# Performance work log

Hardware: AMD Instinct MI355X
Metric: run time of the kernel (lower is better)

Reference implementation:

```python
import jax, jax.numpy as jnp
import numpy as np

EPS = 1e-3  # Keras BatchNormalization default epsilon


def _binarize(x):
    # sign() binarization with straight-through estimator (identity gradient)
    b = jnp.where(x >= 0, 1.0, -1.0).astype(x.dtype)
    return x + jax.lax.stop_gradient(b - x)


def _conv(x, w):
    # NHWC input, HWIO kernel, stride 1, 'same' padding
    return jax.lax.conv_general_dilated(
        x, w, (1, 1), 'SAME', dimension_numbers=('NHWC', 'HWIO', 'NHWC'))


def _bn(x, p):
    # p: [4, C] rows = gamma, beta, moving_mean, moving_var (inference BN)
    gamma, beta, mean, var = p[0], p[1], p[2], p[3]
    return gamma * (x - mean) * jax.lax.rsqrt(var + EPS) + beta


def _maxpool(x):
    return jax.lax.reduce_window(x, -jnp.inf, jax.lax.max,
                                 (1, 2, 2, 1), (1, 2, 2, 1), 'VALID')


def _bconv_block(x, w, bn_p):
    # BinaryConv2D(activation='relu', use_bias=False) -> BatchNormalization
    y = jax.nn.relu(_conv(_binarize(x), _binarize(w)))
    return _bn(y, bn_p)


def setup_inputs() -> dict:
    key = jax.random.key(0)
    ks = iter(jax.random.split(key, 64))

    def w(shape, scale=0.05):
        return jax.random.normal(next(ks), shape, jnp.float32) * scale

    def bn_params(c):
        gamma = 1.0 + 0.1 * jax.random.normal(next(ks), (c,), jnp.float32)
        beta = 0.1 * jax.random.normal(next(ks), (c,), jnp.float32)
        mean = 0.1 * jax.random.normal(next(ks), (c,), jnp.float32)
        var = 0.5 + jax.random.uniform(next(ks), (c,), jnp.float32)
        return jnp.stack([gamma, beta, mean, var])

    inp = {
        'inputs': jax.random.normal(next(ks), (16, 224, 224, 3), jnp.float32),
        'conv1_w': w((3, 3, 3, 64)), 'conv1_b': w((64,)), 'bn1': bn_params(64),
        'w2': w((3, 3, 64, 128)),  'bn2': bn_params(128),
        'w3': w((3, 3, 128, 256)), 'bn3': bn_params(256),
        'w4': w((3, 3, 256, 256)), 'bn4': bn_params(256),
        'w5': w((3, 3, 256, 512)), 'bn5': bn_params(512),
        'w6': w((3, 3, 512, 512)), 'bn6': bn_params(512),
        'w7': w((3, 3, 512, 512)), 'bn7': bn_params(512),
        'w8': w((3, 3, 512, 512)), 'bn8': bn_params(512),
        'dense_w': w((512, 1000)),
    }
    return inp


def reference(inputs, conv1_w, conv1_b, bn1, w2, bn2, w3, bn3, w4, bn4,
              w5, bn5, w6, bn6, w7, bn7, w8, bn8, dense_w):
    # stage 1: full-precision conv -> BN -> maxpool
    x = jax.nn.relu(_conv(inputs, conv1_w) + conv1_b)
    x = _bn(x, bn1)
    x = _maxpool(x)              # 224 -> 112
    x = 0.5 * x                  # Scale(0.5)
    # binary (XNOR) conv stages, stride 1 (use_maxpool=True)
    x = _bconv_block(x, w2, bn2)
    x = _maxpool(x)              # 112 -> 56
    x = _bconv_block(x, w3, bn3)
    x = _bconv_block(x, w4, bn4)
    x = _maxpool(x)              # 56 -> 28
    x = _bconv_block(x, w5, bn5)
    x = _bconv_block(x, w6, bn6)
    x = _maxpool(x)              # 28 -> 14
    x = _bconv_block(x, w7, bn7)
    x = _bconv_block(x, w8, bn8)
    x = _maxpool(x)              # 14 -> 7
    x = jnp.mean(x, axis=(1, 2))  # global average pool -> [B, 512]
    # BinaryDense: binarized input and weights, no bias
    return _binarize(x) @ _binarize(dense_w)
```

## Files before the change

kernel.cpp:

```cpp
#include <hip/hip_runtime.h>
#include <cstdint>

using u64 = unsigned long long;

__global__ void pack_conv_weights(const float* __restrict__ w, u64* __restrict__ wb,
                                  int Cin, int Cout) {
    int cinw = Cin >> 6;
    int total = 9 * cinw * Cout;
    int idx = blockIdx.x * blockDim.x + threadIdx.x;
    if (idx >= total) return;
    int co = idx % Cout;
    int rest = idx / Cout;
    int wd = rest % cinw;
    int t = rest / cinw;
    u64 word = 0ull;
    for (int b = 0; b < 64; ++b) {
        int ci = (wd << 6) + b;
        float v = w[(t * Cin + ci) * Cout + co];
        if (v >= 0.f) word |= (1ull << b);
    }
    wb[idx] = word;
}

__global__ void pack_dense_weights(const float* __restrict__ w, u64* __restrict__ wb) {
    int j = blockIdx.x * blockDim.x + threadIdx.x;
    if (j >= 1000) return;
    for (int wd = 0; wd < 8; ++wd) {
        u64 word = 0ull;
        for (int b = 0; b < 64; ++b) {
            float v = w[((wd << 6) + b) * 1000 + j];
            if (v >= 0.f) word |= (1ull << b);
        }
        wb[j * 8 + wd] = word;
    }
}

__global__ void prep_bnthr(const float* __restrict__ bn, int cout,
                           double* __restrict__ thrd, int* __restrict__ sflag) {
    int i = blockIdx.x * blockDim.x + threadIdx.x;
    if (i >= cout) return;
    double g  = (double)bn[i];
    double be = (double)bn[cout + i];
    double mu = (double)bn[2 * cout + i];
    double va = (double)bn[3 * cout + i];
    double s  = g * (1.0 / sqrt(va + 1e-3));
    thrd[i] = mu - be / s;
    sflag[i] = (s >= 0.0) ? 1 : 0;
}

__global__ void prep_thrf(const double* __restrict__ thrd, float* __restrict__ thrf) {
    int i = threadIdx.x;
    if (i < 64) thrf[i] = (float)thrd[i];
}

__global__ __launch_bounds__(256, 1)
void conv1_fused(const float* __restrict__ in, const float* __restrict__ w,
                 const float* __restrict__ bias,
                 const float* __restrict__ thrf, const double* __restrict__ thrd,
                 const int* __restrict__ sflag,
                 u64* __restrict__ outbits) {
    int lane = threadIdx.x & 63;
    int wid = blockIdx.x * (blockDim.x >> 6) + (threadIdx.x >> 6);
    int pxq = wid % 28;
    int py  = (wid / 28) % 112;
    int n   = wid / (28 * 112);

    float  thrv = thrf[lane];
    double thrD = thrd[lane];
    bool   spos = (sflag[lane] != 0);
    float  bif  = bias[lane];

    float wreg[27];
#pragma unroll
    for (int t = 0; t < 9; ++t)
#pragma unroll
        for (int c = 0; c < 3; ++c)
            wreg[t * 3 + c] = w[(t * 3 + c) * 64 + lane];

    const float TAU = 2e-4f;
    int iy0 = 2 * py - 1;
    bool rowint = (py >= 1) & (py <= 110);

#pragma unroll 1
    for (int pp = 0; pp < 4; ++pp) {
        int px = 4 * pxq + pp;
        int ix0 = 2 * px - 1;

        float patch[4][12];
        bool interior = rowint & (px >= 1) & (px <= 110);
        if (interior) {
            const float* base = in + ((size_t)(n * 224 + iy0) * 224 + ix0) * 3;
#pragma unroll
            for (int r = 0; r < 4; ++r) {
                const float* rp = base + (size_t)r * (224 * 3);
#pragma unroll
                for (int c = 0; c < 12; ++c) patch[r][c] = rp[c];
            }
        } else {
#pragma unroll
            for (int r = 0; r < 4; ++r) {
                int iy = iy0 + r;
                bool rv = (iy >= 0) & (iy < 224);
#pragma unroll
                for (int cc = 0; cc < 4; ++cc) {
                    int ix = ix0 + cc;
                    bool v = rv & (ix >= 0) & (ix < 224);
                    const float* p = in + ((size_t)(n * 224 + iy) * 224 + ix) * 3;
#pragma unroll
                    for (int c = 0; c < 3; ++c)
                        patch[r][cc * 3 + c] = v ? p[c] : 0.f;
                }
            }
        }

        bool pred = false;
#pragma unroll
        for (int q = 0; q < 4; ++q) {
            int qy = q >> 1, qx = q & 1;
            float accf = bif;
#pragma unroll
            for (int dy = 0; dy < 3; ++dy)
#pragma unroll
                for (int dx = 0; dx < 3; ++dx)
#pragma unroll
                    for (int c = 0; c < 3; ++c)
                        accf = fmaf(patch[qy + dy][(qx + dx) * 3 + c],
                                    wreg[(dy * 3 + dx) * 3 + c], accf);
            float rf = fmaxf(accf, 0.f);
            bool p = spos ? (rf >= thrv) : (rf <= thrv);
            if (fabsf(rf - thrv) < TAU) {
                double acc = (double)bif;
#pragma unroll
                for (int dy = 0; dy < 3; ++dy)
#pragma unroll
                    for (int dx = 0; dx < 3; ++dx)
#pragma unroll
                        for (int c = 0; c < 3; ++c)
                            acc = fma((double)patch[qy + dy][(qx + dx) * 3 + c],
                                      (double)wreg[(dy * 3 + dx) * 3 + c], acc);
                double rd = fmax(acc, 0.0);
                p = spos ? (rd >= thrD) : (rd <= thrD);
            }
            pred |= p;
        }
        u64 word = __ballot(pred);
        if (lane == 0) outbits[((size_t)(n * 112 + py)) * 112 + px] = word;
    }
}

template<int CINW, int COUT, int P, bool OUTF64>
__global__ void bconv(const u64* __restrict__ xin, const u64* __restrict__ wb,
                      const float* __restrict__ bn,
                      const double* __restrict__ thrd, const int* __restrict__ sflag,
                      u64* __restrict__ obits, double* __restrict__ of64,
                      int H, int W) {
    constexpr int CW = COUT >> 6;
    __shared__ u64 sh[3][P + 2][CINW];

    int tid = threadIdx.x;
    int XT = (W + P - 1) / P;
    int pos = blockIdx.x;
    int xt = pos % XT;
    int yy = (pos / XT) % H;
    int n  = pos / (XT * H);
    int x0 = xt * P;

    for (int i = tid; i < 3 * (P + 2) * CINW; i += COUT) {
        int wd = i % CINW;
        int cc = (i / CINW) % (P + 2);
        int rr = i / (CINW * (P + 2));
        int gy = yy - 1 + rr, gx = x0 - 1 + cc;
        u64 v = 0ull;
        if (gy >= 0 && gy < H && gx >= 0 && gx < W)
            v = xin[((size_t)(n * H + gy) * W + gx) * CINW + wd];
        sh[rr][cc][wd] = v;
    }
    __syncthreads();

    int acc[P];
#pragma unroll
    for (int p = 0; p < P; ++p) acc[p] = 0;

    int co = tid;
    bool leftv  = (x0 > 0);
    bool rightv = (x0 + P < W);

    for (int dy = 0; dy < 3; ++dy) {
        int gy = yy - 1 + dy;
        if (gy < 0 || gy >= H) continue;
#pragma unroll 1
        for (int w = 0; w < CINW; ++w) {
            u64 w0 = wb[((dy * 3 + 0) * CINW + w) * COUT + co];
            u64 w1 = wb[((dy * 3 + 1) * CINW + w) * COUT + co];
            u64 w2 = wb[((dy * 3 + 2) * CINW + w) * COUT + co];
#pragma unroll
            for (int c = 0; c < P + 2; ++c) {
                if (c == 0 && !leftv) continue;
                if (c == P + 1 && !rightv) continue;
                u64 v = sh[dy][c][w];
                if (c < P)  acc[c]     += __popcll(v ^ w0);
                if (c >= 1 && c <= P) acc[c - 1] += __popcll(v ^ w1);
                if (c >= 2) acc[c - 2] += __popcll(v ^ w2);
            }
        }
    }

    int ndy = 3 - (yy == 0) - (yy == H - 1);
    int lane = tid & 63, wv = tid >> 6;

    if constexpr (OUTF64) {
        double g  = (double)bn[co];
        double be = (double)bn[COUT + co];
        double mu = (double)bn[2 * COUT + co];
        double va = (double)bn[3 * COUT + co];
        double rsq = 1.0 / sqrt(va + 1e-3);
#pragma unroll
        for (int p = 0; p < P; ++p) {
            int x = x0 + p;
            bool eL = (x == 0), eR = (x == W - 1);
            int nvp = ndy * (3 - eL - eR);
            int y = nvp * (CINW * 64) - 2 * acc[p];
            int yr = y > 0 ? y : 0;
            double v = g * ((double)yr - mu) * rsq + be;
            if (x < W) of64[((size_t)(n * H + yy) * W + x) * COUT + co] = v;
        }
    } else {
        double thr = thrd[co];
        bool spos = (sflag[co] != 0);
#pragma unroll
        for (int p = 0; p < P; ++p) {
            int x = x0 + p;
            bool eL = (x == 0), eR = (x == W - 1);
            int nvp = ndy * (3 - eL - eR);
            int y = nvp * (CINW * 64) - 2 * acc[p];
            int yr = y > 0 ? y : 0;
            double yd = (double)yr;
            bool pred = spos ? (yd >= thr) : (yd <= thr);
            u64 word = __ballot(pred);
            if (lane == 0 && x < W)
                obits[((size_t)(n * H + yy) * W + x) * CW + wv] = word;
        }
    }
}

__global__ void pool_bits(const u64* __restrict__ in, u64* __restrict__ out,
                          int H2, int W2, int CW) {
    int idx = blockIdx.x * blockDim.x + threadIdx.x;
    int total = 16 * H2 * W2 * CW;
    if (idx >= total) return;
    int wd = idx % CW;
    int rest = idx / CW;
    int px = rest % W2; rest /= W2;
    int py = rest % H2;
    int n = rest / H2;
    int W = 2 * W2;
    const u64* base = in + ((size_t)(n * 2 * H2 + 2 * py) * W + 2 * px) * CW + wd;
    out[idx] = base[0] | base[CW] | base[(size_t)W * CW] | base[(size_t)W * CW + CW];
}

__global__ void gap_part(const double* __restrict__ x, double* __restrict__ part) {
    int b = blockIdx.x;
    int py = b % 7, n = b / 7;
    int co = threadIdx.x;
    double sum = 0.0;
    for (int px = 0; px < 7; ++px) {
        const double* bp = x + ((size_t)(n * 14 + 2 * py) * 14 + 2 * px) * 512 + co;
        double m = bp[0];
        m = fmax(m, bp[512]);
        m = fmax(m, bp[14 * 512]);
        m = fmax(m, bp[14 * 512 + 512]);
        sum += m;
    }
    part[((size_t)n * 7 + py) * 512 + co] = sum;
}

__global__ void gap_final(const double* __restrict__ part, u64* __restrict__ gb) {
    int n = blockIdx.x;
    int co = threadIdx.x;
    double sum = 0.0;
    for (int py = 0; py < 7; ++py) sum += part[((size_t)n * 7 + py) * 512 + co];
    double mean = sum / 49.0;
    bool pred = (mean >= 0.0);
    u64 word = __ballot(pred);
    if ((co & 63) == 0) gb[n * 8 + (co >> 6)] = word;
}

__global__ void dense_bin(const u64* __restrict__ gb, const u64* __restrict__ dwb,
                          float* __restrict__ out) {
    int idx = blockIdx.x * blockDim.x + threadIdx.x;
    if (idx >= 16000) return;
    int j = idx % 1000, n = idx / 1000;
    const u64* g = gb + n * 8;
    const u64* w = dwb + j * 8;
    int acc = 0;
#pragma unroll
    for (int wd = 0; wd < 8; ++wd) acc += __popcll(g[wd] ^ w[wd]);
    out[idx] = (float)(512 - 2 * acc);
}

extern "C" void kernel_launch(void* const* d_in, const int* in_sizes, int n_in,
                              void* d_out, int out_size, void* d_ws, size_t ws_size,
                              hipStream_t stream) {
    const float* inputs = (const float*)d_in[0];
    const float* w1  = (const float*)d_in[1];
    const float* b1  = (const float*)d_in[2];
    const float* bn1 = (const float*)d_in[3];
    const float* w2  = (const float*)d_in[4];
    const float* bn2 = (const float*)d_in[5];
    const float* w3  = (const float*)d_in[6];
    const float* bn3 = (const float*)d_in[7];
    const float* w4  = (const float*)d_in[8];
    const float* bn4 = (const float*)d_in[9];
    const float* w5  = (const float*)d_in[10];
    const float* bn5 = (const float*)d_in[11];
    const float* w6  = (const float*)d_in[12];
    const float* bn6 = (const float*)d_in[13];
    const float* w7  = (const float*)d_in[14];
    const float* bn7 = (const float*)d_in[15];
    const float* w8  = (const float*)d_in[16];
    const float* bn8 = (const float*)d_in[17];
    const float* dw  = (const float*)d_in[18];
    float* out = (float*)d_out;

    u64* ws = (u64*)d_ws;
    size_t o = 0;
    auto alloc = [&](size_t n) { u64* p = ws + o; o += n; return p; };

    u64* wb2 = alloc(9 * 1 * 128);
    u64* wb3 = alloc(9 * 2 * 256);
    u64* wb4 = alloc(9 * 4 * 256);
    u64* wb5 = alloc(9 * 4 * 512);
    u64* wb6 = alloc(9 * 8 * 512);
    u64* wb7 = alloc(9 * 8 * 512);
    u64* wb8 = alloc(9 * 8 * 512);
    u64* dwb = alloc(1000 * 8);

    double* th1 = (double*)alloc(64);   int* sf1 = (int*)alloc(64);
    double* th2 = (double*)alloc(128);  int* sf2 = (int*)alloc(128);
    double* th3 = (double*)alloc(256);  int* sf3 = (int*)alloc(256);
    double* th4 = (double*)alloc(256);  int* sf4 = (int*)alloc(256);
    double* th5 = (double*)alloc(512);  int* sf5 = (int*)alloc(512);
    double* th6 = (double*)alloc(512);  int* sf6 = (int*)alloc(512);
    double* th7 = (double*)alloc(512);  int* sf7 = (int*)alloc(512);
    float*  tf1 = (float*)alloc(64);

    u64* x2b = alloc(16 * 112 * 112 * 1);
    u64* c2b = alloc(16 * 112 * 112 * 2);
    u64* x3b = alloc(16 * 56 * 56 * 2);
    u64* c3b = alloc(16 * 56 * 56 * 4);
    u64* c4b = alloc(16 * 56 * 56 * 4);
    u64* x5b = alloc(16 * 28 * 28 * 4);
    u64* c5b = alloc(16 * 28 * 28 * 8);
    u64* c6b = alloc(16 * 28 * 28 * 8);
    u64* x7b = alloc(16 * 14 * 14 * 8);
    u64* c7b = alloc(16 * 14 * 14 * 8);
    u64* gb  = alloc(16 * 8);
    double* c8f   = (double*)alloc(16 * 14 * 14 * 512);
    double* gpart = (double*)alloc(16 * 7 * 512);

    auto grid = [](int n, int b) { return (n + b - 1) / b; };
    pack_conv_weights<<<grid(9 * 1 * 128, 256), 256, 0, stream>>>(w2, wb2, 64, 128);
    pack_conv_weights<<<grid(9 * 2 * 256, 256), 256, 0, stream>>>(w3, wb3, 128, 256);
    pack_conv_weights<<<grid(9 * 4 * 256, 256), 256, 0, stream>>>(w4, wb4, 256, 256);
    pack_conv_weights<<<grid(9 * 4 * 512, 256), 256, 0, stream>>>(w5, wb5, 256, 512);
    pack_conv_weights<<<grid(9 * 8 * 512, 256), 256, 0, stream>>>(w6, wb6, 512, 512);
    pack_conv_weights<<<grid(9 * 8 * 512, 256), 256, 0, stream>>>(w7, wb7, 512, 512);
    pack_conv_weights<<<grid(9 * 8 * 512, 256), 256, 0, stream>>>(w8, wb8, 512, 512);
    pack_dense_weights<<<4, 256, 0, stream>>>(dw, dwb);

    prep_bnthr<<<1, 64, 0, stream>>>(bn1, 64, th1, sf1);
    prep_bnthr<<<1, 128, 0, stream>>>(bn2, 128, th2, sf2);
    prep_bnthr<<<1, 256, 0, stream>>>(bn3, 256, th3, sf3);
    prep_bnthr<<<1, 256, 0, stream>>>(bn4, 256, th4, sf4);
    prep_bnthr<<<grid(512, 256), 256, 0, stream>>>(bn5, 512, th5, sf5);
    prep_bnthr<<<grid(512, 256), 256, 0, stream>>>(bn6, 512, th6, sf6);
    prep_bnthr<<<grid(512, 256), 256, 0, stream>>>(bn7, 512, th7, sf7);
    prep_thrf<<<1, 64, 0, stream>>>(th1, tf1);

    conv1_fused<<<16 * 112 * 28 / 4, 256, 0, stream>>>(inputs, w1, b1, tf1, th1, sf1, x2b);

    bconv<1, 128, 8, false><<<16 * 112 * 14, 128, 0, stream>>>(x2b, wb2, bn2, th2, sf2, c2b, nullptr, 112, 112);
    pool_bits<<<grid(16 * 56 * 56 * 2, 256), 256, 0, stream>>>(c2b, x3b, 56, 56, 2);
    bconv<2, 256, 8, false><<<16 * 56 * 7, 256, 0, stream>>>(x3b, wb3, bn3, th3, sf3, c3b, nullptr, 56, 56);
    bconv<4, 256, 8, false><<<16 * 56 * 7, 256, 0, stream>>>(c3b, wb4, bn4, th4, sf4, c4b, nullptr, 56, 56);
    pool_bits<<<grid(16 * 28 * 28 * 4, 256), 256, 0, stream>>>(c4b, x5b, 28, 28, 4);
    bconv<4, 512, 7, false><<<16 * 28 * 4, 512, 0, stream>>>(x5b, wb5, bn5, th5, sf5, c5b, nullptr, 28, 28);
    bconv<8, 512, 7, false><<<16 * 28 * 4, 512, 0, stream>>>(c5b, wb6, bn6, th6, sf6, c6b, nullptr, 28, 28);
    pool_bits<<<grid(16 * 14 * 14 * 8, 256), 256, 0, stream>>>(c6b, x7b, 14, 14, 8);
    bconv<8, 512, 7, false><<<16 * 14 * 2, 512, 0, stream>>>(x7b, wb7, bn7, th7, sf7, c7b, nullptr, 14, 14);
    bconv<8, 512, 7, true><<<16 * 14 * 2, 512, 0, stream>>>(c7b, wb8, bn8, nullptr, nullptr, nullptr, c8f, 14, 14);

    gap_part<<<16 * 7, 512, 0, stream>>>(c8f, gpart);
    gap_final<<<16, 512, 0, stream>>>(gpart, gb);
    dense_bin<<<grid(16000, 256), 256, 0, stream>>>(gb, dwb, out);
}
```

Baseline: 518.4 us.

## Register-block binary conv over two output rows to reuse weight loads

The binary conv kernel now computes R=2 output rows per block, staging R+2 input rows in shared memory and loading all nine weight words per input word once, then reusing them across both rows. This halves the number of weight global loads per output and halves the block count. In exchange it doubles the accumulator registers and the shared tile, which may reduce occupancy. It also assumes H and W divide evenly by R and P, so the x<W guards are dropped.

```diff
diff --git a/kernel.cpp b/kernel.cpp
--- a/kernel.cpp
+++ b/kernel.cpp
@@ -148,28 +148,30 @@
     }
 }
 
-template<int CINW, int COUT, int P, bool OUTF64>
+template<int CINW, int COUT, int P, int R, bool OUTF64>
 __global__ void bconv(const u64* __restrict__ xin, const u64* __restrict__ wb,
                       const float* __restrict__ bn,
                       const double* __restrict__ thrd, const int* __restrict__ sflag,
                       u64* __restrict__ obits, double* __restrict__ of64,
                       int H, int W) {
     constexpr int CW = COUT >> 6;
-    __shared__ u64 sh[3][P + 2][CINW];
+    __shared__ u64 sh[R + 2][P + 2][CINW];
 
     int tid = threadIdx.x;
-    int XT = (W + P - 1) / P;
+    int XT = W / P;
+    int YT = H / R;
     int pos = blockIdx.x;
     int xt = pos % XT;
-    int yy = (pos / XT) % H;
-    int n  = pos / (XT * H);
+    int yt = (pos / XT) % YT;
+    int n  = pos / (XT * YT);
     int x0 = xt * P;
-
-    for (int i = tid; i < 3 * (P + 2) * CINW; i += COUT) {
+    int y0 = yt * R;
+
+    for (int i = tid; i < (R + 2) * (P + 2) * CINW; i += COUT) {
         int wd = i % CINW;
         int cc = (i / CINW) % (P + 2);
         int rr = i / (CINW * (P + 2));
-        int gy = yy - 1 + rr, gx = x0 - 1 + cc;
+        int gy = y0 - 1 + rr, gx = x0 - 1 + cc;
         u64 v = 0ull;
         if (gy >= 0 && gy < H && gx >= 0 && gx < W)
             v = xin[((size_t)(n * H + gy) * W + gx) * CINW + wd];
@@ -177,35 +179,44 @@
     }
     __syncthreads();
 
-    int acc[P];
-#pragma unroll
-    for (int p = 0; p < P; ++p) acc[p] = 0;
+    int acc[R][P];
+#pragma unroll
+    for (int r = 0; r < R; ++r)
+#pragma unroll
+        for (int p = 0; p < P; ++p) acc[r][p] = 0;
 
     int co = tid;
     bool leftv  = (x0 > 0);
     bool rightv = (x0 + P < W);
 
-    for (int dy = 0; dy < 3; ++dy) {
-        int gy = yy - 1 + dy;
-        if (gy < 0 || gy >= H) continue;
 #pragma unroll 1
-        for (int w = 0; w < CINW; ++w) {
-            u64 w0 = wb[((dy * 3 + 0) * CINW + w) * COUT + co];
-            u64 w1 = wb[((dy * 3 + 1) * CINW + w) * COUT + co];
-            u64 w2 = wb[((dy * 3 + 2) * CINW + w) * COUT + co];
+    for (int w = 0; w < CINW; ++w) {
+        u64 wt[9];
+#pragma unroll
+        for (int t = 0; t < 9; ++t)
+            wt[t] = wb[(t * CINW + w) * COUT + co];
+#pragma unroll
+        for (int rr = 0; rr < R + 2; ++rr) {
+            int gy = y0 + rr - 1;
+            if (gy < 0 || gy >= H) continue;
 #pragma unroll
             for (int c = 0; c < P + 2; ++c) {
                 if (c == 0 && !leftv) continue;
                 if (c == P + 1 && !rightv) continue;
-                u64 v = sh[dy][c][w];
-                if (c < P)  acc[c]     += __popcll(v ^ w0);
-                if (c >= 1 && c <= P) acc[c - 1] += __popcll(v ^ w1);
-                if (c >= 2) acc[c - 2] += __popcll(v ^ w2);
-            }
-        }
-    }
-
-    int ndy = 3 - (yy == 0) - (yy == H - 1);
+                u64 v = sh[rr][c][w];
+#pragma unroll
+                for (int r = 0; r < R; ++r) {
+                    constexpr int unused = 0; (void)unused;
+                    int dy = rr - r;
+                    if (dy < 0 || dy > 2) continue;
+                    if (c < P)            acc[r][c]     += __popcll(v ^ wt[dy * 3 + 0]);
+                    if (c >= 1 && c <= P) acc[r][c - 1] += __popcll(v ^ wt[dy * 3 + 1]);
+                    if (c >= 2)           acc[r][c - 2] += __popcll(v ^ wt[dy * 3 + 2]);
+                }
+            }
+        }
+    }
+
     int lane = tid & 63, wv = tid >> 6;
 
     if constexpr (OUTF64) {
@@ -215,30 +226,40 @@
         double va = (double)bn[3 * COUT + co];
         double rsq = 1.0 / sqrt(va + 1e-3);
 #pragma unroll
-        for (int p = 0; p < P; ++p) {
-            int x = x0 + p;
-            bool eL = (x == 0), eR = (x == W - 1);
-            int nvp = ndy * (3 - eL - eR);
-            int y = nvp * (CINW * 64) - 2 * acc[p];
-            int yr = y > 0 ? y : 0;
-            double v = g * ((double)yr - mu) * rsq + be;
-            if (x < W) of64[((size_t)(n * H + yy) * W + x) * COUT + co] = v;
+        for (int r = 0; r < R; ++r) {
+            int yy = y0 + r;
+            int ndy = 3 - (yy == 0) - (yy == H - 1);
+#pragma unroll
+            for (int p = 0; p < P; ++p) {
+                int x = x0 + p;
+                bool eL = (x == 0), eR = (x == W - 1);
+                int nvp = ndy * (3 - eL - eR);
+                int y = nvp * (CINW * 64) - 2 * acc[r][p];
+                int yr = y > 0 ? y : 0;
+                double v = g * ((double)yr - mu) * rsq + be;
+                of64[((size_t)(n * H + yy) * W + x) * COUT + co] = v;
+            }
         }
     } else {
         double thr = thrd[co];
         bool spos = (sflag[co] != 0);
 #pragma unroll
-        for (int p = 0; p < P; ++p) {
-            int x = x0 + p;
-            bool eL = (x == 0), eR = (x == W - 1);
-            int nvp = ndy * (3 - eL - eR);
-            int y = nvp * (CINW * 64) - 2 * acc[p];
-            int yr = y > 0 ? y : 0;
-            double yd = (double)yr;
-            bool pred = spos ? (yd >= thr) : (yd <= thr);
-            u64 word = __ballot(pred);
-            if (lane == 0 && x < W)
-                obits[((size_t)(n * H + yy) * W + x) * CW + wv] = word;
+        for (int r = 0; r < R; ++r) {
+            int yy = y0 + r;
+            int ndy = 3 - (yy == 0) - (yy == H - 1);
+#pragma unroll
+            for (int p = 0; p < P; ++p) {
+                int x = x0 + p;
+                bool eL = (x == 0), eR = (x == W - 1);
+                int nvp = ndy * (3 - eL - eR);
+                int y = nvp * (CINW * 64) - 2 * acc[r][p];
+                int yr = y > 0 ? y : 0;
+                double yd = (double)yr;
+                bool pred = spos ? (yd >= thr) : (yd <= thr);
+                u64 word = __ballot(pred);
+                if (lane == 0)
+                    obits[((size_t)(n * H + yy) * W + x) * CW + wv] = word;
+            }
         }
     }
 }
@@ -379,16 +400,16 @@
 
     conv1_fused<<<16 * 112 * 28 / 4, 256, 0, stream>>>(inputs, w1, b1, tf1, th1, sf1, x2b);
 
-    bconv<1, 128, 8, false><<<16 * 112 * 14, 128, 0, stream>>>(x2b, wb2, bn2, th2, sf2, c2b, nullptr, 112, 112);
+    bconv<1, 128, 8, 2, false><<<16 * 56 * 14, 128, 0, stream>>>(x2b, wb2, bn2, th2, sf2, c2b, nullptr, 112, 112);
     pool_bits<<<grid(16 * 56 * 56 * 2, 256), 256, 0, stream>>>(c2b, x3b, 56, 56, 2);
-    bconv<2, 256, 8, false><<<16 * 56 * 7, 256, 0, stream>>>(x3b, wb3, bn3, th3, sf3, c3b, nullptr, 56, 56);
-    bconv<4, 256, 8, false><<<16 * 56 * 7, 256, 0, stream>>>(c3b, wb4, bn4, th4, sf4, c4b, nullptr, 56, 56);
+    bconv<2, 256, 8, 2, false><<<16 * 28 * 7, 256, 0, stream>>>(x3b, wb3, bn3, th3, sf3, c3b, nullptr, 56, 56);
+    bconv<4, 256, 8, 2, false><<<16 * 28 * 7, 256, 0, stream>>>(c3b, wb4, bn4, th4, sf4, c4b, nullptr, 56, 56);
     pool_bits<<<grid(16 * 28 * 28 * 4, 256), 256, 0, stream>>>(c4b, x5b, 28, 28, 4);
-    bconv<4, 512, 7, false><<<16 * 28 * 4, 512, 0, stream>>>(x5b, wb5, bn5, th5, sf5, c5b, nullptr, 28, 28);
-    bconv<8, 512, 7, false><<<16 * 28 * 4, 512, 0, stream>>>(c5b, wb6, bn6, th6, sf6, c6b, nullptr, 28, 28);
+    bconv<4, 512, 7, 2, false><<<16 * 14 * 4, 512, 0, stream>>>(x5b, wb5, bn5, th5, sf5, c5b, nullptr, 28, 28);
+    bconv<8, 512, 7, 2, false><<<16 * 14 * 4, 512, 0, stream>>>(c5b, wb6, bn6, th6, sf6, c6b, nullptr, 28, 28);
     pool_bits<<<grid(16 * 14 * 14 * 8, 256), 256, 0, stream>>>(c6b, x7b, 14, 14, 8);
-    bconv<8, 512, 7, false><<<16 * 14 * 2, 512, 0, stream>>>(x7b, wb7, bn7, th7, sf7, c7b, nullptr, 14, 14);
-    bconv<8, 512, 7, true><<<16 * 14 * 2, 512, 0, stream>>>(c7b, wb8, bn8, nullptr, nullptr, nullptr, c8f, 14, 14);
+    bconv<8, 512, 7, 2, false><<<16 * 7 * 2, 512, 0, stream>>>(x7b, wb7, bn7, th7, sf7, c7b, nullptr, 14, 14);
+    bconv<8, 512, 7, 2, true><<<16 * 7 * 2, 512, 0, stream>>>(c7b, wb8, bn8, nullptr, nullptr, nullptr, c8f, 14, 14);
 
     gap_part<<<16 * 7, 512, 0, stream>>>(c8f, gpart);
     gap_final<<<16, 512, 0, stream>>>(gpart, gb);
```

After: 535.5 us. 3.3% more time.
